# Kernel tuning notes

Hardware: AMD Instinct MI355X
Metric: run time of the kernel (lower is better)

The kernel has to match this reference:

```python
import jax, jax.numpy as jnp
import numpy as np

B, N, C = 4, 2048, 81
IMG_W, IMG_H = 1024.0, 800.0
SCORE_THRESH = 0.05
NMS_THRESH = 0.5
DETS_PER_IMG = 100
BBOX_XFORM_CLIP = float(np.log(1000.0 / 16.0))
WX, WY, WW, WH = 10.0, 10.0, 5.0, 5.0


def _make_boxes(key, n):
    k1, k2, k3, k4 = jax.random.split(key, 4)
    x1 = jax.random.uniform(k1, (n,)) * (IMG_W - 60.0)
    y1 = jax.random.uniform(k2, (n,)) * (IMG_H - 60.0)
    w = 10.0 + jax.random.uniform(k3, (n,)) * 300.0
    h = 10.0 + jax.random.uniform(k4, (n,)) * 300.0
    return jnp.stack([x1, y1, jnp.minimum(x1 + w, IMG_W - 1.0), jnp.minimum(y1 + h, IMG_H - 1.0)], axis=-1)


def setup_inputs() -> dict:
    key = jax.random.key(0)
    k1, k2, k3, k4 = jax.random.split(key, 4)
    return {
        "class_logits": jax.random.normal(k1, (B * N, C), jnp.float32),
        "box_regression": jax.random.normal(k2, (B * N, C * 8), jnp.float32) * 0.5,
        "left_proposals": _make_boxes(k3, B * N),
        "right_proposals": _make_boxes(k4, B * N),
    }


def decode(rel, boxes):
    widths = boxes[:, 2] - boxes[:, 0] + 1.0
    heights = boxes[:, 3] - boxes[:, 1] + 1.0
    ctr_x = boxes[:, 0] + 0.5 * widths
    ctr_y = boxes[:, 1] + 0.5 * heights
    dx = rel[:, 0::4] / WX
    dy = rel[:, 1::4] / WY
    dw = jnp.minimum(rel[:, 2::4] / WW, BBOX_XFORM_CLIP)
    dh = jnp.minimum(rel[:, 3::4] / WH, BBOX_XFORM_CLIP)
    pcx = dx * widths[:, None] + ctr_x[:, None]
    pcy = dy * heights[:, None] + ctr_y[:, None]
    pw = jnp.exp(dw) * widths[:, None]
    ph = jnp.exp(dh) * heights[:, None]
    x1 = pcx - 0.5 * pw
    y1 = pcy - 0.5 * ph
    x2 = pcx + 0.5 * pw - 1.0
    y2 = pcy + 0.5 * ph - 1.0
    return jnp.stack([x1, y1, x2, y2], axis=-1)  # [M, C, 4]


def clip_boxes(b):
    x1 = jnp.clip(b[..., 0], 0.0, IMG_W - 1.0)
    y1 = jnp.clip(b[..., 1], 0.0, IMG_H - 1.0)
    x2 = jnp.clip(b[..., 2], 0.0, IMG_W - 1.0)
    y2 = jnp.clip(b[..., 3], 0.0, IMG_H - 1.0)
    return jnp.stack([x1, y1, x2, y2], axis=-1)


def pairwise_iou(b):
    area = jnp.clip(b[:, 2] - b[:, 0] + 1.0, 0.0) * jnp.clip(b[:, 3] - b[:, 1] + 1.0, 0.0)
    lt = jnp.maximum(b[:, None, :2], b[None, :, :2])
    rb = jnp.minimum(b[:, None, 2:], b[None, :, 2:])
    wh = jnp.clip(rb - lt + 1.0, 0.0)
    inter = wh[..., 0] * wh[..., 1]
    return inter / jnp.maximum(area[:, None] + area[None, :] - inter, 1e-6)


def nms_keep(boxes, scores):
    # greedy NMS -> boolean keep mask (fixed shape)
    n = scores.shape[0]
    order = jnp.argsort(-scores)
    iou = pairwise_iou(boxes[order])
    idx = jnp.arange(n)
    def body(i, keep):
        sup = (iou[i] > NMS_THRESH) & keep[i] & (idx > i)
        return keep & (~sup)
    keep = jax.lax.fori_loop(0, n, body, jnp.ones((n,), bool))
    return jnp.zeros((n,), bool).at[order].set(keep)


def _per_image(prob, lb, rb):
    # prob [N,C], lb/rb [N,C,4]
    labels = jnp.argmax(prob, axis=-1)
    ar = jnp.arange(prob.shape[0])
    score = prob[ar, labels]
    lbox = lb[ar, labels]
    rbox = rb[ar, labels]
    valid = (labels >= 1) & (score > SCORE_THRESH)
    s = jnp.where(valid, score, -jnp.inf)
    keep = nms_keep(lbox, s) & nms_keep(rbox, s) & valid
    ms = jnp.where(keep, score, -jnp.inf)
    kth = jax.lax.top_k(ms, DETS_PER_IMG)[0][-1]
    keep = keep & (ms >= kth)
    return lbox, rbox, score, keep


def reference(class_logits, box_regression, left_proposals, right_proposals):
    prob = jax.nn.softmax(class_logits, axis=-1)  # [B*N, C]
    reg = box_regression.reshape(-1, C, 8)
    lb = clip_boxes(decode(reg[:, :, :4].reshape(-1, C * 4), left_proposals))
    rb = clip_boxes(decode(reg[:, :, 4:].reshape(-1, C * 4), right_proposals))
    prob = prob.reshape(B, N, C)
    lb = lb.reshape(B, N, C, 4)
    rb = rb.reshape(B, N, C, 4)
    lbox, rbox, score, keep = jax.vmap(_per_image)(prob, lb, rb)
    m = keep[..., None].astype(score.dtype)
    out = jnp.concatenate([lbox * m, rbox * m, jnp.where(keep, score, 0.0)[..., None]], axis=-1)
    return out  # [B, N, 9]
```

## Files before the change

### kernel.cpp

```cpp
#include <hip/hip_runtime.h>
#include <math.h>

#define NPROP 2048
#define NIMG 4
#define NCLS 81
#define REGW 648
#define SCORE_THRESH 0.05f
#define NMS_T 0.5f
#define DETS 100
#define XC 1023.0f
#define YC 799.0f
#define BBOX_CLIP 4.135166556742356f
#define NBIN 8192
#define SEL 320
#define MAXC 512
#define WRD 8
#define TRIP 2560

typedef unsigned long long u64;

__device__ __forceinline__ float areaf(float4 v) {
  return fmaxf(v.z - v.x + 1.0f, 0.0f) * fmaxf(v.w - v.y + 1.0f, 0.0f);
}
__device__ __forceinline__ bool iou_gt(float4 a, float aa, float4 b, float ba) {
  float ix1 = fmaxf(a.x, b.x), iy1 = fmaxf(a.y, b.y);
  float ix2 = fminf(a.z, b.z), iy2 = fminf(a.w, b.w);
  float iw = fmaxf(ix2 - ix1 + 1.0f, 0.0f);
  float ih = fmaxf(iy2 - iy1 + 1.0f, 0.0f);
  float inter = iw * ih;
  return inter > NMS_T * fmaxf(aa + ba - inter, 1e-6f);
}
__device__ __forceinline__ float score_from_v(unsigned v) {
  unsigned uu = ~v;
  unsigned bits = (uu & 0x80000000u) ? (uu & 0x7fffffffu) : ~uu;
  return __uint_as_float(bits);
}
__device__ __forceinline__ float4 decode_side(const float* __restrict__ reg,
                                              const float4* __restrict__ props,
                                              int grow, int ci, int isR) {
  const float* r = reg + (size_t)grow * REGW + ci * 8 + isR * 4;
  float4 P = props[grow];
  float w  = P.z - P.x + 1.0f;
  float h  = P.w - P.y + 1.0f;
  float cx = P.x + 0.5f * w;
  float cy = P.y + 0.5f * h;
  float dx = r[0] / 10.0f;
  float dy = r[1] / 10.0f;
  float dw = fminf(r[2] / 5.0f, BBOX_CLIP);
  float dh = fminf(r[3] / 5.0f, BBOX_CLIP);
  float pcx = dx * w + cx;
  float pcy = dy * h + cy;
  float pw = expf(dw) * w;
  float ph = expf(dh) * h;
  float4 o;
  o.x = fminf(fmaxf(pcx - 0.5f * pw, 0.0f), XC);
  o.y = fminf(fmaxf(pcy - 0.5f * ph, 0.0f), YC);
  o.z = fminf(fmaxf(pcx + 0.5f * pw - 1.0f, 0.0f), XC);
  o.w = fminf(fmaxf(pcy + 0.5f * ph - 1.0f, 0.0f), YC);
  return o;
}

__global__ __launch_bounds__(256) void score_kernel(
    const float* __restrict__ logits,
    unsigned* __restrict__ v32G, unsigned short* __restrict__ ci16G,
    float* __restrict__ out) {
  int row  = blockIdx.x * 4 + (threadIdx.x >> 6);
  int lane = threadIdx.x & 63;
  if (blockIdx.x < 72) {
    int g = blockIdx.x * 256 + threadIdx.x;
    ((float4*)out)[g] = make_float4(0.f, 0.f, 0.f, 0.f);
  }
  const float* lr = logits + (size_t)row * NCLS;
  float a = lr[lane];
  float b = (lane < NCLS - 64) ? lr[lane + 64] : -INFINITY;
  float v; int ci;
  if (b > a) { v = b; ci = lane + 64; } else { v = a; ci = lane; }
  for (int o = 32; o; o >>= 1) {
    float ov = __shfl_xor(v, o);
    int   oc = __shfl_xor(ci, o);
    if (ov > v || (ov == v && oc < ci)) { v = ov; ci = oc; }
  }
  float e = expf(a - v) + ((lane < NCLS - 64) ? expf(b - v) : 0.0f);
  for (int o = 32; o; o >>= 1) e += __shfl_xor(e, o);
  if (lane == 0) {
    float score = 1.0f / e;
    unsigned vv = 0xFFFFFFFFu;
    if (ci >= 1 && score > SCORE_THRESH) {
      unsigned uu = __float_as_uint(score);
      uu = (uu & 0x80000000u) ? ~uu : (uu | 0x80000000u);
      vv = ~uu;
    }
    v32G[row]  = vv;
    ci16G[row] = (unsigned short)ci;
  }
}

__global__ __launch_bounds__(1024) void nms8_kernel(
    const unsigned* __restrict__ v32G, const unsigned short* __restrict__ ci16G,
    const float* __restrict__ reg, const float* __restrict__ lp,
    const float* __restrict__ rp,
    unsigned short* __restrict__ srowG, unsigned* __restrict__ svG,
    float4* __restrict__ bxLG, float4* __restrict__ bxRG,
    u64* __restrict__ keepLG, u64* __restrict__ keepRG,
    int* __restrict__ C1G, int* __restrict__ C2G, int* __restrict__ flagG) {
  __shared__ int hist[NBIN];
  __shared__ u64 keys[MAXC];
  __shared__ unsigned short ssort[MAXC];
  __shared__ float4 bx[MAXC];
  __shared__ u64 mat[TRIP];
  __shared__ int wsum[16];
  __shared__ int Ts, cnts, ovf;
  int b = blockIdx.x >> 1, side = blockIdx.x & 1;
  int tid = threadIdx.x, ln = tid & 63, w = tid >> 6;
  const unsigned* v32 = v32G + b * NPROP;
  if (tid == 0) { Ts = NBIN - 1; cnts = 0; ovf = 0; }
  for (int i = tid; i < NBIN; i += 1024) hist[i] = 0;
  __syncthreads();
  for (int p = tid; p < NPROP; p += 1024) {
    unsigned v = v32[p];
    if (v != 0xFFFFFFFFu) atomicAdd(&hist[v >> 19], 1);
  }
  __syncthreads();
  {
    int base = tid * 8;
    int c[8]; int acc = 0;
#pragma unroll
    for (int k = 0; k < 8; ++k) { acc += hist[base + k]; c[k] = acc; }
    int tot = acc, v = tot;
#pragma unroll
    for (int o = 1; o < 64; o <<= 1) { int n = __shfl_up(v, o); if (ln >= o) v += n; }
    if (ln == 63) wsum[w] = v;
    __syncthreads();
    if (tid < 16) {
      int x = wsum[tid];
#pragma unroll
      for (int o = 1; o < 16; o <<= 1) { int n = __shfl_up(x, o); if (tid >= o) x += n; }
      wsum[tid] = x;
    }
    __syncthreads();
    int incl = ((w > 0) ? wsum[w - 1] : 0) + v;
    int off = incl - tot;
    int prev = off;
#pragma unroll
    for (int k = 0; k < 8; ++k) {
      int cur = off + c[k];
      if (cur >= SEL && prev < SEL) Ts = base + k;
      prev = cur;
    }
  }
  __syncthreads();
  int T = Ts, nvTot = wsum[15];
  for (int p = tid; p < NPROP; p += 1024) {
    unsigned v = v32[p];
    bool cand = (v != 0xFFFFFFFFu) && ((int)(v >> 19) <= T);
    u64 mb = __ballot(cand);
    int lpos = (int)__popcll(mb & ((1ull << ln) - 1ull));
    int wb = 0;
    if (ln == 0 && mb) wb = atomicAdd(&cnts, (int)__popcll(mb));
    wb = __shfl(wb, 0);
    if (cand) {
      int dst = wb + lpos;
      if (dst < MAXC) keys[dst] = ((u64)v << 16) | (unsigned)p;
      else ovf = 1;
    }
  }
  __syncthreads();
  int C1 = cnts;
  if (C1 > MAXC || ovf) {
    if (tid == 0) { flagG[b] = 1; C1G[b] = 0; C2G[b] = nvTot; }
    return;
  }
  if (tid == 0) { flagG[b] = 0; C1G[b] = C1; C2G[b] = nvTot; }
  if (tid < 256) {
    int i0 = tid, i1 = tid + 256;
    u64 k0 = (i0 < C1) ? keys[i0] : ~0ull;
    u64 k1 = (i1 < C1) ? keys[i1] : ~0ull;
    int r0 = 0, r1 = 0;
#pragma unroll 4
    for (int j = 0; j < C1; ++j) {
      u64 kj = keys[j];
      r0 += (kj < k0) ? 1 : 0;
      r1 += (kj < k1) ? 1 : 0;
    }
    if (i0 < C1) {
      unsigned short rw = (unsigned short)(k0 & 0xFFFFull);
      ssort[r0] = rw;
      srowG[b * MAXC + r0] = rw;
      svG[b * MAXC + r0]   = (unsigned)(k0 >> 16);
    }
    if (i1 < C1) {
      unsigned short rw = (unsigned short)(k1 & 0xFFFFull);
      ssort[r1] = rw;
      srowG[b * MAXC + r1] = rw;
      svG[b * MAXC + r1]   = (unsigned)(k1 >> 16);
    }
  }
  __syncthreads();

  int WRDu = (C1 + 63) >> 6;
  if (tid < MAXC) {
    float4 B = make_float4(0.f, 0.f, 0.f, 0.f);
    if (tid < C1) {
      int row  = ssort[tid];
      int grow = b * NPROP + row;
      int ci   = ci16G[grow];
      B = decode_side(reg, (const float4*)(side ? rp : lp), grow, ci, side);
      (side ? bxRG : bxLG)[b * MAXC + tid] = B;
    }
    bx[tid] = B;
  }
  __syncthreads();

  {
    int rb = w & 7, part = w >> 3;
    int r = rb * 64 + ln;
    float4 rbx = bx[r];
    float  rar = areaf(rbx);
    int tb = 0;
    for (int k = 0; k < rb; ++k) tb += ((8 - k) | 1);
    int Sw = (8 - rb) | 1;
    u64* myrow = &mat[tb * 64 + ln * Sw];
    for (int cw = rb + part; cw < WRDu; cw += 2) {
      u64 m = 0;
      const float4* cp = &bx[cw * 64];
#pragma unroll 8
      for (int c = 0; c < 64; ++c) {
        float4 cb = cp[c];
        float car = areaf(cb);
        if (iou_gt(rbx, rar, cb, car)) m |= (1ull << c);
      }
      if (cw == rb) m &= ~((2ull << ln) - 1ull);
      myrow[cw - rb] = m;
    }
  }
  __syncthreads();

  if (w == 0) {
    u64 A[WRD];
#pragma unroll
    for (int t = 0; t < WRD; ++t) {
      int b0 = t * 64;
      A[t] = (C1 >= b0 + 64) ? ~0ull : (C1 > b0 ? ((1ull << (C1 - b0)) - 1ull) : 0ull);
    }
    int tbase = 0;
#pragma unroll
    for (int wb = 0; wb < WRD; ++wb) {
      if (wb * 64 < C1) {
        const int Sw = (8 - wb) | 1;
        const u64* rowp = &mat[tbase];
        u64 aw = A[wb];
#pragma unroll
        for (int g = 0; g < 4; ++g) {
          u64 d[16];
#pragma unroll
          for (int k = 0; k < 16; ++k) d[k] = rowp[(g * 16 + k) * Sw];
#pragma unroll
          for (int k = 0; k < 16; ++k) {
            u64 msk = 0ull - ((aw >> (g * 16 + k)) & 1ull);
            aw &= ~(msk & d[k]);
          }
        }
        A[wb] = aw;
        bool alive = (aw >> ln) & 1ull;
#pragma unroll
        for (int t = wb + 1; t < WRD; ++t) {
          if (t * 64 < C1) {
            u64 x = alive ? rowp[ln * Sw + (t - wb)] : 0ull;
#pragma unroll
            for (int o = 1; o < 64; o <<= 1)
              x |= __shfl_xor((unsigned long long)x, o);
            A[t] &= ~x;
          }
        }
      }
      tbase += 64 * ((8 - wb) | 1);
    }
    if (ln == 0) {
      u64* kG = (side ? keepRG : keepLG) + b * WRD;
#pragma unroll
      for (int t = 0; t < WRD; ++t)
        if (t * 64 < C1) kG[t] = A[t];
    }
  }
}

struct SN {
  u64 keys[NPROP];
  unsigned short sidx[NPROP];
  unsigned v32s[NPROP];
  float4 bxL[MAXC], bxR[MAXC];
  float  arL[MAXC], arR[MAXC];
  u64 keepbL[NPROP / 64], keepbR[NPROP / 64];
  u64 rowmL[64], rowmR[64];
  float4 cbL[64], cbR[64];
  float  cbLa[64], cbRa[64];
  u64 aL, aR;
  int cnt, prevCount, done, ccL, ccR, needFB;
  unsigned kthV;
};

__device__ __forceinline__ float4 get_sboxN(SN* S, const float* reg,
                                            const float4* lp4, const float4* rp4,
                                            const unsigned short* ci16G,
                                            int b, int pos, int isR) {
  if (pos < MAXC) return isR ? S->bxR[pos] : S->bxL[pos];
  int row = S->sidx[pos];
  int grow = b * NPROP + row;
  return decode_side(reg, isR ? rp4 : lp4, grow, ci16G[grow], isR);
}

__global__ __launch_bounds__(1024) void finale_fallback_kernel(
    const float* __restrict__ reg, const float* __restrict__ lp,
    const float* __restrict__ rp, const unsigned* __restrict__ v32G,
    const unsigned short* __restrict__ ci16G,
    const u64* __restrict__ keepLG, const u64* __restrict__ keepRG,
    const unsigned* __restrict__ svG, const unsigned short* __restrict__ srowG,
    const float4* __restrict__ bxLG, const float4* __restrict__ bxRG,
    const int* __restrict__ C1G, const int* __restrict__ C2G,
    float* __restrict__ out) {
  __shared__ SN S;
  int b = blockIdx.x, tid = threadIdx.x, ln = tid & 63, w = tid >> 6;
  float* ob = out + (size_t)b * NPROP * 9;

  if (w == 0) {
    int C1 = C1G[b];
    int before = 0;
    unsigned kth = 0;
    for (int wb = 0; wb * 64 < C1; ++wb) {
      u64 m = keepLG[b * WRD + wb] & keepRG[b * WRD + wb];
      int pos = wb * 64 + ln;
      bool bit = (m >> ln) & 1ull;
      int rank = before + (int)__popcll(m & ((1ull << ln) - 1ull));
      unsigned vA = svG[b * MAXC + pos];
      u64 selm = __ballot(bit && rank == DETS - 1);
      if (selm) kth = __shfl(vA, __ffsll(selm) - 1);
      bool qual = bit && (rank < DETS || vA == kth);
      if (qual) {
        int row = srowG[b * MAXC + pos];
        float4 L = bxLG[b * MAXC + pos], R = bxRG[b * MAXC + pos];
        float* orow = ob + row * 9;
        orow[0]=L.x; orow[1]=L.y; orow[2]=L.z; orow[3]=L.w;
        orow[4]=R.x; orow[5]=R.y; orow[6]=R.z; orow[7]=R.w;
        orow[8]=score_from_v(vA);
      }
      before += (int)__popcll(m);
    }
    if (ln == 0) {
      S.needFB = (before < DETS && C2G[b] > C1) ? 1 : 0;
      S.cnt = 0; S.prevCount = 0; S.done = 0; S.kthV = 0u;
    }
  }
  __syncthreads();
  if (!S.needFB) return;

  const float4* lp4 = (const float4*)lp;
  const float4* rp4 = (const float4*)rp;
  float4* ob4 = (float4*)ob;
  float4 z4 = make_float4(0.f, 0.f, 0.f, 0.f);
  for (int i = tid; i < NPROP * 9 / 4; i += 1024) ob4[i] = z4;
  for (int p = tid; p < NPROP; p += 1024) {
    unsigned v = v32G[b * NPROP + p];
    S.v32s[p] = v;
    bool cand = (v != 0xFFFFFFFFu);
    u64 mb = __ballot(cand);
    int lpos = (int)__popcll(mb & ((1ull << ln) - 1ull));
    int wb = 0;
    if (ln == 0 && mb) wb = atomicAdd(&S.cnt, (int)__popcll(mb));
    wb = __shfl(wb, 0);
    if (cand) S.keys[wb + lpos] = ((u64)v << 16) | (unsigned)p;
  }
  __syncthreads();
  int C2 = S.cnt;
  int CbEnd = (C2 + 63) & ~63;
  {
    int i0 = tid, i1 = tid + 1024;
    u64 k0 = (i0 < C2) ? S.keys[i0] : ~0ull;
    u64 k1 = (i1 < C2) ? S.keys[i1] : ~0ull;
    int r0 = 0, r1 = 0;
#pragma unroll 4
    for (int j = 0; j < C2; ++j) {
      u64 kj = S.keys[j];
      r0 += (kj < k0) ? 1 : 0;
      r1 += (kj < k1) ? 1 : 0;
    }
    if (i0 < C2) S.sidx[r0] = (unsigned short)(k0 & 0xFFFFull);
    if (i1 < C2) S.sidx[r1] = (unsigned short)(k1 & 0xFFFFull);
  }
  for (int i = C2 + tid; i < CbEnd; i += 1024) S.sidx[i] = 0;
  for (int wd = tid; wd < NPROP / 64; wd += 1024) {
    int b0 = wd << 6;
    u64 mf = 0ull;
    if (C2 >= b0 + 64) mf = ~0ull;
    else if (C2 > b0)  mf = (1ull << (C2 - b0)) - 1ull;
    S.keepbL[wd] = mf; S.keepbR[wd] = mf;
  }
  __syncthreads();
  {
    int lim = min(CbEnd, MAXC);
    for (int i = tid; i < lim; i += 1024) {
      if (i < C2) {
        int row = S.sidx[i];
        int grow = b * NPROP + row;
        int ci = ci16G[grow];
        float4 L = decode_side(reg, lp4, grow, ci, 0);
        float4 R = decode_side(reg, lp4 == rp4 ? lp4 : rp4, grow, ci, 1);
        S.bxL[i] = L; S.arL[i] = areaf(L);
        S.bxR[i] = R; S.arR[i] = areaf(R);
      } else {
        S.bxL[i] = z4; S.arL[i] = 1.0f;
        S.bxR[i] = z4; S.arR[i] = 1.0f;
      }
    }
  }
  __syncthreads();
  for (int base = 0; base < CbEnd; base += 64) {
    {
      int isR = (w >= 8);
      float4 cbx = get_sboxN(&S, reg, lp4, rp4, ci16G, b, base + ln, isR);
      float car = (base + ln < MAXC) ? (isR ? S.arR[base + ln] : S.arL[base + ln])
                                     : areaf(cbx);
      int w8 = w & 7;
#pragma unroll
      for (int k = 0; k < 8; ++k) {
        int row = w8 * 8 + k;
        float4 rbx;
        rbx.x = __shfl(cbx.x, row); rbx.y = __shfl(cbx.y, row);
        rbx.z = __shfl(cbx.z, row); rbx.w = __shfl(cbx.w, row);
        float rar = __shfl(car, row);
        bool bit = (ln > row) && iou_gt(rbx, rar, cbx, car);
        u64 bal = __ballot(bit);
        if (ln == 0) { if (isR) S.rowmR[row] = bal; else S.rowmL[row] = bal; }
      }
    }
    __syncthreads();
    if (tid < 128) {
      int isR = (tid >= 64);
      u64* km = isR ? S.keepbR : S.keepbL;
      u64* rm = isR ? S.rowmR  : S.rowmL;
      u64 a = km[base >> 6];
#pragma unroll
      for (int j = 0; j < 64; ++j)
        a &= ~((0ull - ((a >> j) & 1ull)) & rm[j]);
      if (ln == 0) {
        km[base >> 6] = a;
        if (isR) { S.aR = a; S.ccR = __popcll(a); }
        else     { S.aL = a; S.ccL = __popcll(a); }
      }
      if ((a >> ln) & 1ull) {
        int pos = __popcll(a & ((1ull << ln) - 1ull));
        float4 v = get_sboxN(&S, reg, lp4, rp4, ci16G, b, base + ln, isR);
        if (isR) { S.cbR[pos] = v; S.cbRa[pos] = areaf(v); }
        else     { S.cbL[pos] = v; S.cbLa[pos] = areaf(v); }
      }
    }
    __syncthreads();
    if (w == 0) {
      u64 m = S.aL & S.aR;
      int before = S.prevCount;
      bool bit = (m >> ln) & 1ull;
      int rank = before + (int)__popcll(m & ((1ull << ln) - 1ull));
      int row = S.sidx[base + ln];
      unsigned vA = S.v32s[row];
      u64 selm = __ballot(bit && rank == DETS - 1);
      unsigned keffV = S.kthV;
      if (selm) keffV = __shfl(vA, __ffsll(selm) - 1);
      bool qual = bit && (rank < DETS || vA == keffV);
      if (qual) {
        float4 L = get_sboxN(&S, reg, lp4, rp4, ci16G, b, base + ln, 0);
        float4 R = get_sboxN(&S, reg, lp4, rp4, ci16G, b, base + ln, 1);
        float s = score_from_v(vA);
        float* orow = ob + row * 9;
        orow[0]=L.x; orow[1]=L.y; orow[2]=L.z; orow[3]=L.w;
        orow[4]=R.x; orow[5]=R.y; orow[6]=R.z; orow[7]=R.w;
        orow[8]=s;
      }
      if (ln == 0) {
        if (selm) S.kthV = keffV;
        int nc = before + (int)__popcll(m);
        S.prevCount = nc;
        if (nc >= DETS) {
          int nxt = base + 64;
          bool cont = false;
          if (nxt < C2) cont = (S.v32s[S.sidx[nxt]] == keffV);
          if (!cont) S.done = 1;
        }
      }
    } else {
      int cL = S.ccL, cR = S.ccR;
      if ((cL | cR) != 0) {
        for (int p = base + 64 + (tid - 64); p < CbEnd; p += 960) {
          float4 mbL = get_sboxN(&S, reg, lp4, rp4, ci16G, b, p, 0);
          float al = (p < MAXC) ? S.arL[p] : areaf(mbL);
          bool supL = false;
          for (int q = 0; q < cL; ++q)
            supL = supL || iou_gt(mbL, al, S.cbL[q], S.cbLa[q]);
          if (supL) atomicAnd(&S.keepbL[p >> 6], ~(1ull << (p & 63)));
          float4 mbR = get_sboxN(&S, reg, lp4, rp4, ci16G, b, p, 1);
          float ar_ = (p < MAXC) ? S.arR[p] : areaf(mbR);
          bool supR = false;
          for (int q = 0; q < cR; ++q)
            supR = supR || iou_gt(mbR, ar_, S.cbR[q], S.cbRa[q]);
          if (supR) atomicAnd(&S.keepbR[p >> 6], ~(1ull << (p & 63)));
        }
      }
    }
    __syncthreads();
    if (S.done) break;
  }
}

extern "C" void kernel_launch(void* const* d_in, const int* in_sizes, int n_in,
                              void* d_out, int out_size, void* d_ws, size_t ws_size,
                              hipStream_t stream) {
  const float* logits = (const float*)d_in[0];
  const float* reg    = (const float*)d_in[1];
  const float* lprop  = (const float*)d_in[2];
  const float* rprop  = (const float*)d_in[3];
  float* out = (float*)d_out;

  char* ws = (char*)d_ws;
  unsigned*       v32G   = (unsigned*)(ws + 0);
  unsigned short* ci16G  = (unsigned short*)(ws + 32768);
  unsigned short* srowG  = (unsigned short*)(ws + 49152);
  unsigned*       svG    = (unsigned*)(ws + 53248);
  float4*         bxLG   = (float4*)(ws + 61440);
  float4*         bxRG   = (float4*)(ws + 94208);
  u64*            keepLG = (u64*)(ws + 126976);
  u64*            keepRG = (u64*)(ws + 127232);
  int*            C1G    = (int*)(ws + 127488);
  int*            C2G    = (int*)(ws + 127504);
  int*            flagG  = (int*)(ws + 127520);

  score_kernel<<<NIMG * NPROP / 4, 256,  0, stream>>>(logits, v32G, ci16G, out);
  nms8_kernel <<<2 * NIMG,         1024, 0, stream>>>(v32G, ci16G, reg, lprop, rprop,
                                                      srowG, svG, bxLG, bxRG,
                                                      keepLG, keepRG, C1G, C2G, flagG);
  finale_fallback_kernel<<<NIMG,   1024, 0, stream>>>(reg, lprop, rprop, v32G, ci16G,
                                                      keepLG, keepRG, svG, srowG,
                                                      bxLG, bxRG, C1G, C2G, out);
}
```

Baseline: 121.9 us.

## Fuse score, NMS and finale kernels into one cooperative grid-synced kernel

Merges the three kernel launches into a single cooperative kernel of 8 blocks that uses grid.sync() between the scoring, per-side NMS and finale stages. Shared memory is reused through a union of the stage structs. The aim is to remove launch gaps between kernels. In exchange, the softmax/argmax scoring stage, which used 2048 blocks, now runs on only 8 blocks of 1024 threads. Each wave processes 64 rows serially, so that stage loses most of its parallelism.

```diff
diff --git a/kernel.cpp b/kernel.cpp
--- a/kernel.cpp
+++ b/kernel.cpp
@@ -1,5 +1,8 @@
 #include <hip/hip_runtime.h>
+#include <hip/hip_cooperative_groups.h>
 #include <math.h>
+
+namespace cg = cooperative_groups;
 
 #define NPROP 2048
 #define NIMG 4
@@ -60,229 +63,15 @@
   return o;
 }
 
-__global__ __launch_bounds__(256) void score_kernel(
-    const float* __restrict__ logits,
-    unsigned* __restrict__ v32G, unsigned short* __restrict__ ci16G,
-    float* __restrict__ out) {
-  int row  = blockIdx.x * 4 + (threadIdx.x >> 6);
-  int lane = threadIdx.x & 63;
-  if (blockIdx.x < 72) {
-    int g = blockIdx.x * 256 + threadIdx.x;
-    ((float4*)out)[g] = make_float4(0.f, 0.f, 0.f, 0.f);
-  }
-  const float* lr = logits + (size_t)row * NCLS;
-  float a = lr[lane];
-  float b = (lane < NCLS - 64) ? lr[lane + 64] : -INFINITY;
-  float v; int ci;
-  if (b > a) { v = b; ci = lane + 64; } else { v = a; ci = lane; }
-  for (int o = 32; o; o >>= 1) {
-    float ov = __shfl_xor(v, o);
-    int   oc = __shfl_xor(ci, o);
-    if (ov > v || (ov == v && oc < ci)) { v = ov; ci = oc; }
-  }
-  float e = expf(a - v) + ((lane < NCLS - 64) ? expf(b - v) : 0.0f);
-  for (int o = 32; o; o >>= 1) e += __shfl_xor(e, o);
-  if (lane == 0) {
-    float score = 1.0f / e;
-    unsigned vv = 0xFFFFFFFFu;
-    if (ci >= 1 && score > SCORE_THRESH) {
-      unsigned uu = __float_as_uint(score);
-      uu = (uu & 0x80000000u) ? ~uu : (uu | 0x80000000u);
-      vv = ~uu;
-    }
-    v32G[row]  = vv;
-    ci16G[row] = (unsigned short)ci;
-  }
-}
-
-__global__ __launch_bounds__(1024) void nms8_kernel(
-    const unsigned* __restrict__ v32G, const unsigned short* __restrict__ ci16G,
-    const float* __restrict__ reg, const float* __restrict__ lp,
-    const float* __restrict__ rp,
-    unsigned short* __restrict__ srowG, unsigned* __restrict__ svG,
-    float4* __restrict__ bxLG, float4* __restrict__ bxRG,
-    u64* __restrict__ keepLG, u64* __restrict__ keepRG,
-    int* __restrict__ C1G, int* __restrict__ C2G, int* __restrict__ flagG) {
-  __shared__ int hist[NBIN];
-  __shared__ u64 keys[MAXC];
-  __shared__ unsigned short ssort[MAXC];
-  __shared__ float4 bx[MAXC];
-  __shared__ u64 mat[TRIP];
-  __shared__ int wsum[16];
-  __shared__ int Ts, cnts, ovf;
-  int b = blockIdx.x >> 1, side = blockIdx.x & 1;
-  int tid = threadIdx.x, ln = tid & 63, w = tid >> 6;
-  const unsigned* v32 = v32G + b * NPROP;
-  if (tid == 0) { Ts = NBIN - 1; cnts = 0; ovf = 0; }
-  for (int i = tid; i < NBIN; i += 1024) hist[i] = 0;
-  __syncthreads();
-  for (int p = tid; p < NPROP; p += 1024) {
-    unsigned v = v32[p];
-    if (v != 0xFFFFFFFFu) atomicAdd(&hist[v >> 19], 1);
-  }
-  __syncthreads();
-  {
-    int base = tid * 8;
-    int c[8]; int acc = 0;
-#pragma unroll
-    for (int k = 0; k < 8; ++k) { acc += hist[base + k]; c[k] = acc; }
-    int tot = acc, v = tot;
-#pragma unroll
-    for (int o = 1; o < 64; o <<= 1) { int n = __shfl_up(v, o); if (ln >= o) v += n; }
-    if (ln == 63) wsum[w] = v;
-    __syncthreads();
-    if (tid < 16) {
-      int x = wsum[tid];
-#pragma unroll
-      for (int o = 1; o < 16; o <<= 1) { int n = __shfl_up(x, o); if (tid >= o) x += n; }
-      wsum[tid] = x;
-    }
-    __syncthreads();
-    int incl = ((w > 0) ? wsum[w - 1] : 0) + v;
-    int off = incl - tot;
-    int prev = off;
-#pragma unroll
-    for (int k = 0; k < 8; ++k) {
-      int cur = off + c[k];
-      if (cur >= SEL && prev < SEL) Ts = base + k;
-      prev = cur;
-    }
-  }
-  __syncthreads();
-  int T = Ts, nvTot = wsum[15];
-  for (int p = tid; p < NPROP; p += 1024) {
-    unsigned v = v32[p];
-    bool cand = (v != 0xFFFFFFFFu) && ((int)(v >> 19) <= T);
-    u64 mb = __ballot(cand);
-    int lpos = (int)__popcll(mb & ((1ull << ln) - 1ull));
-    int wb = 0;
-    if (ln == 0 && mb) wb = atomicAdd(&cnts, (int)__popcll(mb));
-    wb = __shfl(wb, 0);
-    if (cand) {
-      int dst = wb + lpos;
-      if (dst < MAXC) keys[dst] = ((u64)v << 16) | (unsigned)p;
-      else ovf = 1;
-    }
-  }
-  __syncthreads();
-  int C1 = cnts;
-  if (C1 > MAXC || ovf) {
-    if (tid == 0) { flagG[b] = 1; C1G[b] = 0; C2G[b] = nvTot; }
-    return;
-  }
-  if (tid == 0) { flagG[b] = 0; C1G[b] = C1; C2G[b] = nvTot; }
-  if (tid < 256) {
-    int i0 = tid, i1 = tid + 256;
-    u64 k0 = (i0 < C1) ? keys[i0] : ~0ull;
-    u64 k1 = (i1 < C1) ? keys[i1] : ~0ull;
-    int r0 = 0, r1 = 0;
-#pragma unroll 4
-    for (int j = 0; j < C1; ++j) {
-      u64 kj = keys[j];
-      r0 += (kj < k0) ? 1 : 0;
-      r1 += (kj < k1) ? 1 : 0;
-    }
-    if (i0 < C1) {
-      unsigned short rw = (unsigned short)(k0 & 0xFFFFull);
-      ssort[r0] = rw;
-      srowG[b * MAXC + r0] = rw;
-      svG[b * MAXC + r0]   = (unsigned)(k0 >> 16);
-    }
-    if (i1 < C1) {
-      unsigned short rw = (unsigned short)(k1 & 0xFFFFull);
-      ssort[r1] = rw;
-      srowG[b * MAXC + r1] = rw;
-      svG[b * MAXC + r1]   = (unsigned)(k1 >> 16);
-    }
-  }
-  __syncthreads();
-
-  int WRDu = (C1 + 63) >> 6;
-  if (tid < MAXC) {
-    float4 B = make_float4(0.f, 0.f, 0.f, 0.f);
-    if (tid < C1) {
-      int row  = ssort[tid];
-      int grow = b * NPROP + row;
-      int ci   = ci16G[grow];
-      B = decode_side(reg, (const float4*)(side ? rp : lp), grow, ci, side);
-      (side ? bxRG : bxLG)[b * MAXC + tid] = B;
-    }
-    bx[tid] = B;
-  }
-  __syncthreads();
-
-  {
-    int rb = w & 7, part = w >> 3;
-    int r = rb * 64 + ln;
-    float4 rbx = bx[r];
-    float  rar = areaf(rbx);
-    int tb = 0;
-    for (int k = 0; k < rb; ++k) tb += ((8 - k) | 1);
-    int Sw = (8 - rb) | 1;
-    u64* myrow = &mat[tb * 64 + ln * Sw];
-    for (int cw = rb + part; cw < WRDu; cw += 2) {
-      u64 m = 0;
-      const float4* cp = &bx[cw * 64];
-#pragma unroll 8
-      for (int c = 0; c < 64; ++c) {
-        float4 cb = cp[c];
-        float car = areaf(cb);
-        if (iou_gt(rbx, rar, cb, car)) m |= (1ull << c);
-      }
-      if (cw == rb) m &= ~((2ull << ln) - 1ull);
-      myrow[cw - rb] = m;
-    }
-  }
-  __syncthreads();
-
-  if (w == 0) {
-    u64 A[WRD];
-#pragma unroll
-    for (int t = 0; t < WRD; ++t) {
-      int b0 = t * 64;
-      A[t] = (C1 >= b0 + 64) ? ~0ull : (C1 > b0 ? ((1ull << (C1 - b0)) - 1ull) : 0ull);
-    }
-    int tbase = 0;
-#pragma unroll
-    for (int wb = 0; wb < WRD; ++wb) {
-      if (wb * 64 < C1) {
-        const int Sw = (8 - wb) | 1;
-        const u64* rowp = &mat[tbase];
-        u64 aw = A[wb];
-#pragma unroll
-        for (int g = 0; g < 4; ++g) {
-          u64 d[16];
-#pragma unroll
-          for (int k = 0; k < 16; ++k) d[k] = rowp[(g * 16 + k) * Sw];
-#pragma unroll
-          for (int k = 0; k < 16; ++k) {
-            u64 msk = 0ull - ((aw >> (g * 16 + k)) & 1ull);
-            aw &= ~(msk & d[k]);
-          }
-        }
-        A[wb] = aw;
-        bool alive = (aw >> ln) & 1ull;
-#pragma unroll
-        for (int t = wb + 1; t < WRD; ++t) {
-          if (t * 64 < C1) {
-            u64 x = alive ? rowp[ln * Sw + (t - wb)] : 0ull;
-#pragma unroll
-            for (int o = 1; o < 64; o <<= 1)
-              x |= __shfl_xor((unsigned long long)x, o);
-            A[t] &= ~x;
-          }
-        }
-      }
-      tbase += 64 * ((8 - wb) | 1);
-    }
-    if (ln == 0) {
-      u64* kG = (side ? keepRG : keepLG) + b * WRD;
-#pragma unroll
-      for (int t = 0; t < WRD; ++t)
-        if (t * 64 < C1) kG[t] = A[t];
-    }
-  }
-}
+struct P2S {
+  int hist[NBIN];
+  u64 keys[MAXC];
+  unsigned short ssort[MAXC];
+  float4 bx[MAXC];
+  u64 mat[TRIP];
+  int wsum[16];
+  int Ts, cnts, ovf;
+};
 
 struct SN {
   u64 keys[NPROP];
@@ -309,17 +98,236 @@
   return decode_side(reg, isR ? rp4 : lp4, grow, ci16G[grow], isR);
 }
 
-__global__ __launch_bounds__(1024) void finale_fallback_kernel(
-    const float* __restrict__ reg, const float* __restrict__ lp,
-    const float* __restrict__ rp, const unsigned* __restrict__ v32G,
-    const unsigned short* __restrict__ ci16G,
-    const u64* __restrict__ keepLG, const u64* __restrict__ keepRG,
-    const unsigned* __restrict__ svG, const unsigned short* __restrict__ srowG,
-    const float4* __restrict__ bxLG, const float4* __restrict__ bxRG,
-    const int* __restrict__ C1G, const int* __restrict__ C2G,
+__global__ __launch_bounds__(1024) void mega_kernel(
+    const float* __restrict__ logits, const float* __restrict__ reg,
+    const float* __restrict__ lp, const float* __restrict__ rp,
+    unsigned* __restrict__ v32G, unsigned short* __restrict__ ci16G,
+    unsigned short* __restrict__ srowG, unsigned* __restrict__ svG,
+    float4* __restrict__ bxLG, float4* __restrict__ bxRG,
+    u64* __restrict__ keepLG, u64* __restrict__ keepRG,
+    int* __restrict__ C1G, int* __restrict__ C2G, int* __restrict__ flagG,
     float* __restrict__ out) {
-  __shared__ SN S;
-  int b = blockIdx.x, tid = threadIdx.x, ln = tid & 63, w = tid >> 6;
+  cg::grid_group grid = cg::this_grid();
+  constexpr unsigned SMEM = (sizeof(P2S) > sizeof(SN)) ? sizeof(P2S) : sizeof(SN);
+  __shared__ __align__(16) char smemRaw[SMEM];
+  P2S& P = *reinterpret_cast<P2S*>(smemRaw);
+  SN&  S = *reinterpret_cast<SN*>(smemRaw);
+
+  int tid = threadIdx.x, ln = tid & 63, w = tid >> 6;
+  int bimg = blockIdx.x >> 1, side = blockIdx.x & 1;
+
+  {
+    float4 z4 = make_float4(0.f, 0.f, 0.f, 0.f);
+    for (int g = blockIdx.x * 1024 + tid; g < NIMG * NPROP * 9 / 4; g += 8192)
+      ((float4*)out)[g] = z4;
+    int gw = blockIdx.x * 16 + w;
+#pragma unroll 2
+    for (int rr = 0; rr < 64; ++rr) {
+      int row = gw * 64 + rr;
+      const float* lr = logits + (size_t)row * NCLS;
+      float fa = lr[ln];
+      float fb = (ln < NCLS - 64) ? lr[ln + 64] : -INFINITY;
+      float v; int ci;
+      if (fb > fa) { v = fb; ci = ln + 64; } else { v = fa; ci = ln; }
+      for (int o = 32; o; o >>= 1) {
+        float ov = __shfl_xor(v, o);
+        int   oc = __shfl_xor(ci, o);
+        if (ov > v || (ov == v && oc < ci)) { v = ov; ci = oc; }
+      }
+      float e = expf(fa - v) + ((ln < NCLS - 64) ? expf(fb - v) : 0.0f);
+      for (int o = 32; o; o >>= 1) e += __shfl_xor(e, o);
+      if (ln == 0) {
+        float score = 1.0f / e;
+        unsigned vv = 0xFFFFFFFFu;
+        if (ci >= 1 && score > SCORE_THRESH) {
+          unsigned uu = __float_as_uint(score);
+          uu = (uu & 0x80000000u) ? ~uu : (uu | 0x80000000u);
+          vv = ~uu;
+        }
+        v32G[row]  = vv;
+        ci16G[row] = (unsigned short)ci;
+      }
+    }
+  }
+  grid.sync();
+
+  {
+    const unsigned* v32 = v32G + bimg * NPROP;
+    if (tid == 0) { P.Ts = NBIN - 1; P.cnts = 0; P.ovf = 0; }
+    for (int i = tid; i < NBIN; i += 1024) P.hist[i] = 0;
+    __syncthreads();
+    for (int p = tid; p < NPROP; p += 1024) {
+      unsigned v = v32[p];
+      if (v != 0xFFFFFFFFu) atomicAdd(&P.hist[v >> 19], 1);
+    }
+    __syncthreads();
+    {
+      int base = tid * 8;
+      int c[8]; int acc = 0;
+#pragma unroll
+      for (int k = 0; k < 8; ++k) { acc += P.hist[base + k]; c[k] = acc; }
+      int tot = acc, v = tot;
+#pragma unroll
+      for (int o = 1; o < 64; o <<= 1) { int n = __shfl_up(v, o); if (ln >= o) v += n; }
+      if (ln == 63) P.wsum[w] = v;
+      __syncthreads();
+      if (tid < 16) {
+        int x = P.wsum[tid];
+#pragma unroll
+        for (int o = 1; o < 16; o <<= 1) { int n = __shfl_up(x, o); if (tid >= o) x += n; }
+        P.wsum[tid] = x;
+      }
+      __syncthreads();
+      int incl = ((w > 0) ? P.wsum[w - 1] : 0) + v;
+      int off = incl - tot;
+      int prev = off;
+#pragma unroll
+      for (int k = 0; k < 8; ++k) {
+        int cur = off + c[k];
+        if (cur >= SEL && prev < SEL) P.Ts = base + k;
+        prev = cur;
+      }
+    }
+    __syncthreads();
+    int T = P.Ts, nvTot = P.wsum[15];
+    for (int p = tid; p < NPROP; p += 1024) {
+      unsigned v = v32[p];
+      bool cand = (v != 0xFFFFFFFFu) && ((int)(v >> 19) <= T);
+      u64 mb = __ballot(cand);
+      int lpos = (int)__popcll(mb & ((1ull << ln) - 1ull));
+      int wb = 0;
+      if (ln == 0 && mb) wb = atomicAdd(&P.cnts, (int)__popcll(mb));
+      wb = __shfl(wb, 0);
+      if (cand) {
+        int dst = wb + lpos;
+        if (dst < MAXC) P.keys[dst] = ((u64)v << 16) | (unsigned)p;
+        else P.ovf = 1;
+      }
+    }
+    __syncthreads();
+    int C1 = P.cnts;
+    bool skip = (C1 > MAXC) || P.ovf;
+    if (skip) {
+      if (tid == 0) { flagG[bimg] = 1; C1G[bimg] = 0; C2G[bimg] = nvTot; }
+    } else {
+      if (tid == 0) { flagG[bimg] = 0; C1G[bimg] = C1; C2G[bimg] = nvTot; }
+      if (tid < 256) {
+        int i0 = tid, i1 = tid + 256;
+        u64 k0 = (i0 < C1) ? P.keys[i0] : ~0ull;
+        u64 k1 = (i1 < C1) ? P.keys[i1] : ~0ull;
+        int r0 = 0, r1 = 0;
+#pragma unroll 4
+        for (int j = 0; j < C1; ++j) {
+          u64 kj = P.keys[j];
+          r0 += (kj < k0) ? 1 : 0;
+          r1 += (kj < k1) ? 1 : 0;
+        }
+        if (i0 < C1) {
+          unsigned short rw = (unsigned short)(k0 & 0xFFFFull);
+          P.ssort[r0] = rw;
+          srowG[bimg * MAXC + r0] = rw;
+          svG[bimg * MAXC + r0]   = (unsigned)(k0 >> 16);
+        }
+        if (i1 < C1) {
+          unsigned short rw = (unsigned short)(k1 & 0xFFFFull);
+          P.ssort[r1] = rw;
+          srowG[bimg * MAXC + r1] = rw;
+          svG[bimg * MAXC + r1]   = (unsigned)(k1 >> 16);
+        }
+      }
+      __syncthreads();
+
+      int WRDu = (C1 + 63) >> 6;
+      if (tid < MAXC) {
+        float4 B = make_float4(0.f, 0.f, 0.f, 0.f);
+        if (tid < C1) {
+          int row  = P.ssort[tid];
+          int grow = bimg * NPROP + row;
+          int ci   = ci16G[grow];
+          B = decode_side(reg, (const float4*)(side ? rp : lp), grow, ci, side);
+          (side ? bxRG : bxLG)[bimg * MAXC + tid] = B;
+        }
+        P.bx[tid] = B;
+      }
+      __syncthreads();
+
+      {
+        int rb = w & 7, part = w >> 3;
+        int r = rb * 64 + ln;
+        float4 rbx = P.bx[r];
+        float  rar = areaf(rbx);
+        int tb = 0;
+        for (int k = 0; k < rb; ++k) tb += ((8 - k) | 1);
+        int Sw = (8 - rb) | 1;
+        u64* myrow = &P.mat[tb * 64 + ln * Sw];
+        for (int cw = rb + part; cw < WRDu; cw += 2) {
+          u64 m = 0;
+          const float4* cp = &P.bx[cw * 64];
+#pragma unroll 8
+          for (int c = 0; c < 64; ++c) {
+            float4 cb = cp[c];
+            float car = areaf(cb);
+            if (iou_gt(rbx, rar, cb, car)) m |= (1ull << c);
+          }
+          if (cw == rb) m &= ~((2ull << ln) - 1ull);
+          myrow[cw - rb] = m;
+        }
+      }
+      __syncthreads();
+
+      if (w == 0) {
+        u64 A[WRD];
+#pragma unroll
+        for (int t = 0; t < WRD; ++t) {
+          int b0 = t * 64;
+          A[t] = (C1 >= b0 + 64) ? ~0ull : (C1 > b0 ? ((1ull << (C1 - b0)) - 1ull) : 0ull);
+        }
+        int tbase = 0;
+#pragma unroll
+        for (int wb = 0; wb < WRD; ++wb) {
+          if (wb * 64 < C1) {
+            const int Sw = (8 - wb) | 1;
+            const u64* rowp = &P.mat[tbase];
+            u64 aw = A[wb];
+#pragma unroll
+            for (int g = 0; g < 4; ++g) {
+              u64 d[16];
+#pragma unroll
+              for (int k = 0; k < 16; ++k) d[k] = rowp[(g * 16 + k) * Sw];
+#pragma unroll
+              for (int k = 0; k < 16; ++k) {
+                u64 msk = 0ull - ((aw >> (g * 16 + k)) & 1ull);
+                aw &= ~(msk & d[k]);
+              }
+            }
+            A[wb] = aw;
+            bool alive = (aw >> ln) & 1ull;
+#pragma unroll
+            for (int t = wb + 1; t < WRD; ++t) {
+              if (t * 64 < C1) {
+                u64 x = alive ? rowp[ln * Sw + (t - wb)] : 0ull;
+#pragma unroll
+                for (int o = 1; o < 64; o <<= 1)
+                  x |= __shfl_xor((unsigned long long)x, o);
+                A[t] &= ~x;
+              }
+            }
+          }
+          tbase += 64 * ((8 - wb) | 1);
+        }
+        if (ln == 0) {
+          u64* kG = (side ? keepRG : keepLG) + bimg * WRD;
+#pragma unroll
+          for (int t = 0; t < WRD; ++t)
+            if (t * 64 < C1) kG[t] = A[t];
+        }
+      }
+    }
+  }
+  grid.sync();
+
+  if (side != 0) return;
+  int b = bimg;
   float* ob = out + (size_t)b * NPROP * 9;
 
   if (w == 0) {
@@ -531,11 +539,12 @@
   int*            C2G    = (int*)(ws + 127504);
   int*            flagG  = (int*)(ws + 127520);
 
-  score_kernel<<<NIMG * NPROP / 4, 256,  0, stream>>>(logits, v32G, ci16G, out);
-  nms8_kernel <<<2 * NIMG,         1024, 0, stream>>>(v32G, ci16G, reg, lprop, rprop,
-                                                      srowG, svG, bxLG, bxRG,
-                                                      keepLG, keepRG, C1G, C2G, flagG);
-  finale_fallback_kernel<<<NIMG,   1024, 0, stream>>>(reg, lprop, rprop, v32G, ci16G,
-                                                      keepLG, keepRG, svG, srowG,
-                                                      bxLG, bxRG, C1G, C2G, out);
-}
+  void* args[] = {
+    (void*)&logits, (void*)&reg, (void*)&lprop, (void*)&rprop,
+    (void*)&v32G, (void*)&ci16G, (void*)&srowG, (void*)&svG,
+    (void*)&bxLG, (void*)&bxRG, (void*)&keepLG, (void*)&keepRG,
+    (void*)&C1G, (void*)&C2G, (void*)&flagG, (void*)&out
+  };
+  hipLaunchCooperativeKernel((void*)mega_kernel, dim3(2 * NIMG), dim3(1024),
+                             args, 0, stream);
+}
```

Result: slower. 224.1 us (+83.8%).
